# Performance work log

Measured on AMD Instinct MI355X. Metric: run time of the kernel, lower is better.

## Reference

```python
import jax, jax.numpy as jnp
import numpy as np

NUM_GROUPS = 32
EPS = 1e-6


def group_norm(x, gamma, beta):
    # x: [b, c, h, w]
    b, c, h, w = x.shape
    g = NUM_GROUPS
    xg = x.reshape(b, g, c // g, h, w)
    mean = xg.mean(axis=(2, 3, 4), keepdims=True)
    var = xg.var(axis=(2, 3, 4), keepdims=True)
    xn = ((xg - mean) * jax.lax.rsqrt(var + EPS)).reshape(b, c, h, w)
    return xn * gamma[None, :, None, None] + beta[None, :, None, None]


def conv1x1(x, w, b):
    # x: [b, c, h, w], w: [out_c, in_c], b: [out_c]
    return jnp.einsum('bchw,oc->bohw', x, w) + b[None, :, None, None]


def setup_inputs() -> dict:
    key = jax.random.key(0)
    ks = jax.random.split(key, 11)
    B, C, H, W = 4, 512, 64, 64
    s = 1.0 / np.sqrt(C)
    inp = {
        'x': jax.random.normal(ks[0], (B, C, H, W), dtype=jnp.float32),
        'gn_gamma': jnp.ones((C,), dtype=jnp.float32),
        'gn_beta': jnp.zeros((C,), dtype=jnp.float32),
        'wq': jax.random.normal(ks[1], (C, C), dtype=jnp.float32) * s,
        'bq': jax.random.normal(ks[2], (C,), dtype=jnp.float32) * 0.01,
        'wk': jax.random.normal(ks[3], (C, C), dtype=jnp.float32) * s,
        'bk': jax.random.normal(ks[4], (C,), dtype=jnp.float32) * 0.01,
        'wv': jax.random.normal(ks[5], (C, C), dtype=jnp.float32) * s,
        'bv': jax.random.normal(ks[6], (C,), dtype=jnp.float32) * 0.01,
        'wo': jax.random.normal(ks[7], (C, C), dtype=jnp.float32) * s,
        'bo': jax.random.normal(ks[8], (C,), dtype=jnp.float32) * 0.01,
    }
    return inp


def reference(x, gn_gamma, gn_beta, wq, bq, wk, bk, wv, bv, wo, bo):
    b, c, h, w = x.shape
    h_ = group_norm(x, gn_gamma, gn_beta)
    q = conv1x1(h_, wq, bq).reshape(b, c, h * w)  # [b, c, n]
    k = conv1x1(h_, wk, bk).reshape(b, c, h * w)
    v = conv1x1(h_, wv, bv).reshape(b, c, h * w)
    scale = jnp.asarray(c, x.dtype) ** -0.5
    # attn[b, i, j] = softmax_j(q_i . k_j * scale)
    attn = jax.nn.softmax(jnp.einsum('bci,bcj->bij', q, k) * scale, axis=-1)
    # A[b, c, i] = sum_j attn[b, i, j] * v[b, c, j]
    A = jnp.einsum('bij,bcj->bci', attn, v).reshape(b, c, h, w)
    A = conv1x1(A, wo, bo)
    # NOTE: the original module multiplies (not adds) the input by the attention output
    return x * A
```

## Files before the change

### kernel.cpp

```cpp
#include <hip/hip_runtime.h>
#include <hip/hip_bf16.h>
#include <stdint.h>

typedef __bf16 bf16x8 __attribute__((ext_vector_type(8)));
typedef __bf16 bf16x4 __attribute__((ext_vector_type(4)));
typedef float f32x4 __attribute__((ext_vector_type(4)));

__device__ __forceinline__ void gload_lds16(const __bf16* g, __bf16* l) {
  __builtin_amdgcn_global_load_lds(
      (const __attribute__((address_space(1))) void*)g,
      (__attribute__((address_space(3))) void*)l, 16, 0, 0);
}

__global__ __launch_bounds__(256) void cvt4_kernel(const float* __restrict__ s0,
                                                   const float* __restrict__ s1,
                                                   const float* __restrict__ s2,
                                                   const float* __restrict__ s3,
                                                   __bf16* __restrict__ dst) {
  int i = blockIdx.x * 256 + threadIdx.x;
  const float* srcs[4] = {s0, s1, s2, s3};
  int m = i >> 18;
  dst[i] = (__bf16)srcs[m][i & 262143];
}

__global__ __launch_bounds__(256) void biascat_kernel(const float* __restrict__ bq,
                                                      const float* __restrict__ bk,
                                                      float* __restrict__ bqk) {
  int i = blockIdx.x * 256 + threadIdx.x;
  bqk[i] = (i < 512) ? bq[i] : bk[i - 512];
}

__global__ __launch_bounds__(256) void gn1a_kernel(const float* __restrict__ x,
                                                   __bf16* __restrict__ xbf,
                                                   float2* __restrict__ part) {
  const int tid = threadIdx.x;
  const size_t base4 = ((size_t)blockIdx.x * 8192) >> 2;
  const float4* x4 = (const float4*)x;
  bf16x4* o4 = (bf16x4*)xbf;

  float s1 = 0.f, s2 = 0.f;
#pragma unroll
  for (int j = 0; j < 8; ++j) {
    float4 t = x4[base4 + tid + j * 256];
    s1 += t.x + t.y + t.z + t.w;
    s2 += t.x * t.x + t.y * t.y + t.z * t.z + t.w * t.w;
    bf16x4 o;
    o[0] = (__bf16)t.x; o[1] = (__bf16)t.y; o[2] = (__bf16)t.z; o[3] = (__bf16)t.w;
    o4[base4 + tid + j * 256] = o;
  }
#pragma unroll
  for (int off = 32; off; off >>= 1) {
    s1 += __shfl_xor(s1, off);
    s2 += __shfl_xor(s2, off);
  }
  __shared__ float r1[4], r2[4];
  if ((tid & 63) == 0) { r1[tid >> 6] = s1; r2[tid >> 6] = s2; }
  __syncthreads();
  if (tid == 0)
    part[blockIdx.x] = float2{r1[0] + r1[1] + r1[2] + r1[3],
                              r2[0] + r2[1] + r2[2] + r2[3]};
}

__global__ __launch_bounds__(512) void gn1b_kernel(const float2* __restrict__ part,
                                                   const float* __restrict__ gamma,
                                                   const float* __restrict__ beta,
                                                   float2* __restrict__ gmbt) {
  const int b = blockIdx.x;
  const int t = threadIdx.x;
  __shared__ float sm[32], si[32];
  if (t < 32) {
    float s1 = 0.f, s2 = 0.f;
#pragma unroll
    for (int j = 0; j < 8; ++j) {
      float2 p = part[(b * 32 + t) * 8 + j];
      s1 += p.x; s2 += p.y;
    }
    const float mean = s1 * (1.f / 65536.f);
    const float var = s2 * (1.f / 65536.f) - mean * mean;
    sm[t] = mean;
    si[t] = rsqrtf(var + 1e-6f);
  }
  __syncthreads();
  const int g = t >> 4;
  const float gm = gamma[t] * si[g];
  gmbt[b * 512 + t] = float2{gm, beta[t] - sm[g] * gm};
}

__global__ __launch_bounds__(256) void gn2_kernel(const __bf16* __restrict__ xbf,
                                                  const float2* __restrict__ gmbt,
                                                  __bf16* __restrict__ hnT) {
  const int b = blockIdx.z;
  const int c0 = blockIdx.y * 64;
  const int n0 = blockIdx.x * 64;
  const int t = threadIdx.x;
  __shared__ __bf16 tile[64][72];

  {
    const int row = t >> 2;
    const int col = (t & 3) * 16;
    const __bf16* src = xbf + ((size_t)(b * 512 + c0 + row)) * 4096 + n0 + col;
    bf16x8 u0 = *(const bf16x8*)src;
    bf16x8 u1 = *(const bf16x8*)(src + 8);
    *(bf16x8*)&tile[row][col] = u0;
    *(bf16x8*)&tile[row][col + 8] = u1;
  }
  __syncthreads();
  {
    const int nrow = t >> 2;
    const int cc = (t & 3) * 16;
    bf16x8 o0, o1;
#pragma unroll
    for (int j = 0; j < 16; ++j) {
      const int c = c0 + cc + j;
      float2 s = gmbt[b * 512 + c];
      float val = (float)tile[cc + j][nrow] * s.x + s.y;
      if (j < 8) o0[j] = (__bf16)val; else o1[j - 8] = (__bf16)val;
    }
    __bf16* dst = hnT + ((size_t)b * 4096 + n0 + nrow) * 512 + c0 + cc;
    *(bf16x8*)dst = o0;
    *(bf16x8*)(dst + 8) = o1;
  }
}

__global__ __launch_bounds__(256) void rowsum_inv_kernel(const __bf16* __restrict__ P,
                                                         float* __restrict__ inv) {
  const int r = blockIdx.x * 4 + (threadIdx.x >> 6);
  const int lane = threadIdx.x & 63;
  const bf16x8* rp = (const bf16x8*)(P + (size_t)r * 4096);
  float s = 0.f;
#pragma unroll
  for (int j = 0; j < 8; ++j) {
    bf16x8 v = rp[lane + j * 64];
#pragma unroll
    for (int e = 0; e < 8; ++e) s += (float)v[e];
  }
#pragma unroll
  for (int off = 32; off; off >>= 1) s += __shfl_xor(s, off);
  if (lane == 0) inv[r] = 1.0f / s;
}

template <int BIAS, int EEXP, int RSCALE, int KC>
__global__ __launch_bounds__(512) void gemm6r_kernel(
    const __bf16* __restrict__ A, int lda, long long sA,
    const __bf16* __restrict__ Bm, int ldb, long long sB,
    __bf16* __restrict__ Out, int ldo, long long sO,
    const float* __restrict__ bias, const float* __restrict__ rowinv,
    float scale) {
  constexpr int ASLOT = 8192;
  constexpr int BSLOT = 4096;
  constexpr int WN = 32;
  constexpr int BST = WN + 8;
  __shared__ __bf16 sm[6 * ASLOT + 6 * BSLOT];
  __bf16* smB = sm + 6 * ASLOT;

  const int gx = gridDim.x, gxy = gx * gridDim.y;
  const int nwg = gxy * gridDim.z;
  int bid = blockIdx.x + gx * blockIdx.y + gxy * blockIdx.z;
  bid = (bid & 7) * (nwg >> 3) + (bid >> 3);
  const int bz = bid / gxy;
  const int rem = bid - bz * gxy;
  const int by = rem / gx, bx = rem - by * gx;
  const int tm0 = by * 256, tn0 = bx * 128;

  const int t = threadIdx.x;
  const int lane = t & 63, wid = t >> 6;
  const int wr = wid >> 2, wc = wid & 3;

  const __bf16* Az = A + (size_t)bz * sA;
  const __bf16* Bz = Bm + (size_t)bz * sB;

  const int scol = ((t & 3) * 8) ^ (((t >> 3) & 3) * 8);
  const __bf16* gA0 = Az + (size_t)(tm0 + (t >> 2)) * lda + scol;
  const __bf16* gA1 = gA0 + (size_t)128 * lda;
  const __bf16* gB0 = Bz + (size_t)(tn0 + (t >> 2)) * ldb + scol;
  __bf16* dA = sm + t * 8;
  __bf16* dB = smB + t * 8;

  auto stageA = [&](int ks, int sl) {
    gload_lds16(gA0 + (size_t)ks * 32, dA + sl * ASLOT);
    gload_lds16(gA1 + (size_t)ks * 32, dA + sl * ASLOT + 4096);
  };
  auto stageB = [&](int ks, int sl) {
    gload_lds16(gB0 + (size_t)ks * 32, dB + sl * BSLOT);
  };

  const int lr = lane & 15;
  const int kb = ((lane >> 4) * 16) ^ ((lr & 6) << 3);
  const __bf16* rdA = sm + (((wr * 128 + lr) * 64 + kb) >> 1);
  const __bf16* rdB = smB + (((wc * WN + lr) * 64 + kb) >> 1);

  f32x4 acc[8][2];
#pragma unroll
  for (int m = 0; m < 8; ++m) {
    acc[m][0] = f32x4{0.f, 0.f, 0.f, 0.f};
    acc[m][1] = f32x4{0.f, 0.f, 0.f, 0.f};
  }
  bf16x8 av[8];

  auto rdAfr = [&](int sl) {
#pragma unroll
    for (int m = 0; m < 8; ++m)
      av[m] = *(const bf16x8*)(rdA + sl * ASLOT + m * 512);
  };
  auto mmaPh = [&](int sl, int nh) {
    bf16x8 bv = *(const bf16x8*)(rdB + sl * BSLOT + nh * 512);
    __builtin_amdgcn_s_barrier();
    __builtin_amdgcn_s_setprio(1);
#pragma unroll
    for (int m = 0; m < 8; ++m)
      acc[m][nh] = __builtin_amdgcn_mfma_f32_16x16x32_bf16(av[m], bv, acc[m][nh], 0, 0, 0);
    __builtin_amdgcn_s_setprio(0);
    __builtin_amdgcn_s_barrier();
  };

  constexpr int TOT = KC / 32;

  stageA(0, 0); stageB(0, 0);
  stageA(1, 1); stageB(1, 1);
  stageA(2, 2); stageB(2, 2);
  stageA(3, 3); stageB(3, 3);
  stageA(4, 4); stageB(4, 4);
  asm volatile("s_waitcnt vmcnt(12)" ::: "memory");
  __builtin_amdgcn_s_barrier();

  int cs = 0;
  int ss = 5;
#pragma unroll 1
  for (int s = 0; s < TOT - 5; ++s) {
    rdAfr(cs); stageA(s + 5, ss);   mmaPh(cs, 0);
    stageB(s + 5, ss);
    asm volatile("s_waitcnt vmcnt(12)" ::: "memory");
    mmaPh(cs, 1);
    cs = (cs == 5) ? 0 : cs + 1;
    ss = (ss == 5) ? 0 : ss + 1;
  }
  rdAfr(cs); mmaPh(cs, 0);
  asm volatile("s_waitcnt vmcnt(9)" ::: "memory");
  mmaPh(cs, 1); cs = (cs == 5) ? 0 : cs + 1;
  rdAfr(cs); mmaPh(cs, 0);
  asm volatile("s_waitcnt vmcnt(6)" ::: "memory");
  mmaPh(cs, 1); cs = (cs == 5) ? 0 : cs + 1;
  rdAfr(cs); mmaPh(cs, 0);
  asm volatile("s_waitcnt vmcnt(3)" ::: "memory");
  mmaPh(cs, 1); cs = (cs == 5) ? 0 : cs + 1;
  rdAfr(cs); mmaPh(cs, 0);
  asm volatile("s_waitcnt vmcnt(0)" ::: "memory");
  mmaPh(cs, 1); cs = (cs == 5) ? 0 : cs + 1;
  rdAfr(cs); mmaPh(cs, 0);
  mmaPh(cs, 1);

  __bf16* bnc = sm + wid * 16 * BST;
  const int q4 = (lane >> 4) * 4;
  const int row0 = tm0 + wr * 128;
  const int wn = tn0 + wc * WN;
  float bcol[2];
  bcol[0] = BIAS ? bias[wn + lr] : 0.f;
  bcol[1] = BIAS ? bias[wn + 16 + lr] : 0.f;
#pragma unroll
  for (int m = 0; m < 8; ++m) {
    float ri[4];
    if constexpr (RSCALE) {
#pragma unroll
      for (int r = 0; r < 4; ++r)
        ri[r] = rowinv[(size_t)bz * 4096 + row0 + m * 16 + q4 + r];
    }
#pragma unroll
    for (int n = 0; n < 2; ++n)
#pragma unroll
      for (int r = 0; r < 4; ++r) {
        float val = acc[m][n][r] * scale + bcol[n];
        if constexpr (EEXP) val = exp2f(val * 1.44269504f);
        if constexpr (RSCALE) val *= ri[r];
        bnc[(q4 + r) * BST + n * 16 + lr] = (__bf16)val;
      }
    const int rr = lane >> 2, c8 = (lane & 3) * 8;
    bf16x8 v0 = *(const bf16x8*)&bnc[rr * BST + c8];
    __bf16* op = Out + (size_t)bz * sO +
                 (size_t)(row0 + m * 16 + rr) * ldo + wn + c8;
    *(bf16x8*)op = v0;
  }
}

template <int EPI, int BIAS>
__global__ __launch_bounds__(256) void gemm_lds_kernel(
    const __bf16* __restrict__ A, int lda, long long sA,
    const __bf16* __restrict__ Bm, int ldb, long long sB,
    void* __restrict__ Out, int ldo, long long sO,
    const float* __restrict__ bias, const __bf16* __restrict__ xmul,
    long long sX, float scale, int K) {
  __shared__ __bf16 sTa[2][128 * 32];
  __shared__ __bf16 sTb[2][128 * 32];

  const int gx = gridDim.x, gxy = gx * gridDim.y;
  const int nwg = gxy * gridDim.z;
  int bid = blockIdx.x + gx * blockIdx.y + gxy * blockIdx.z;
  if ((nwg & 7) == 0) bid = (bid & 7) * (nwg >> 3) + (bid >> 3);
  const int bz = bid / gxy;
  const int rem = bid - bz * gxy;
  const int by = rem / gx;
  const int bx = rem - by * gx;

  const int tid = threadIdx.x;
  const int lane = tid & 63;
  const int wid = tid >> 6;
  const int wr = wid >> 1, wc = wid & 1;
  const int tm0 = by * 128, tn0 = bx * 128;
  const int lr = lane & 15, lk = (lane >> 4) * 8;

  const int ch0 = wid * 2;
  const int srow = lane >> 2;
  const int scol = (lane & 3) * 8;
  const __bf16* gA0 = A + (size_t)bz * sA + (size_t)(tm0 + ch0 * 16 + srow) * lda + scol;
  const __bf16* gB0 = Bm + (size_t)bz * sB + (size_t)(tn0 + ch0 * 16 + srow) * ldb + scol;
  const size_t stepA = (size_t)16 * lda, stepB = (size_t)16 * ldb;

  f32x4 acc[4][4];
#pragma unroll
  for (int i = 0; i < 4; ++i)
#pragma unroll
    for (int j = 0; j < 4; ++j) acc[i][j] = f32x4{0.f, 0.f, 0.f, 0.f};

  const int T = K >> 5;
  gload_lds16(gA0, &sTa[0][ch0 * 512]);
  gload_lds16(gA0 + stepA, &sTa[0][ch0 * 512 + 512]);
  gload_lds16(gB0, &sTb[0][ch0 * 512]);
  gload_lds16(gB0 + stepB, &sTb[0][ch0 * 512 + 512]);

  for (int tt = 0; tt < T; ++tt) {
    __syncthreads();
    const int cur = tt & 1;
    if (tt + 1 < T) {
      const __bf16* a = gA0 + (size_t)(tt + 1) * 32;
      const __bf16* b = gB0 + (size_t)(tt + 1) * 32;
      gload_lds16(a, &sTa[cur ^ 1][ch0 * 512]);
      gload_lds16(a + stepA, &sTa[cur ^ 1][ch0 * 512 + 512]);
      gload_lds16(b, &sTb[cur ^ 1][ch0 * 512]);
      gload_lds16(b + stepB, &sTb[cur ^ 1][ch0 * 512 + 512]);
    }
    const __bf16* fa = &sTa[cur][(wr * 64 + lr) * 32 + lk];
    const __bf16* fb = &sTb[cur][(wc * 64 + lr) * 32 + lk];
    bf16x8 a[4], b[4];
#pragma unroll
    for (int i = 0; i < 4; ++i) a[i] = *(const bf16x8*)(fa + i * 512);
#pragma unroll
    for (int j = 0; j < 4; ++j) b[j] = *(const bf16x8*)(fb + j * 512);
#pragma unroll
    for (int i = 0; i < 4; ++i)
#pragma unroll
      for (int j = 0; j < 4; ++j)
        acc[i][j] = __builtin_amdgcn_mfma_f32_16x16x32_bf16(a[i], b[j], acc[i][j], 0, 0, 0);
  }

  const int wm = tm0 + wr * 64, wn = tn0 + wc * 64;
#pragma unroll
  for (int i = 0; i < 4; ++i) {
#pragma unroll
    for (int r = 0; r < 4; ++r) {
      const int row = wm + i * 16 + (lane >> 4) * 4 + r;
#pragma unroll
      for (int j = 0; j < 4; ++j) {
        const int col = wn + j * 16 + lr;
        float val = acc[i][j][r] * scale;
        if (BIAS == 1) val += bias[col];
        if (BIAS == 2) val += bias[row];
        const size_t off = (size_t)bz * sO + (size_t)row * ldo + col;
        if (EPI == 0) {
          ((__bf16*)Out)[off] = (__bf16)val;
        } else if (EPI == 1) {
          ((float*)Out)[off] = val;
        } else {
          ((float*)Out)[off] = (float)xmul[(size_t)bz * sX + (size_t)row * ldo + col] * val;
        }
      }
    }
  }
}

extern "C" void kernel_launch(void* const* d_in, const int* in_sizes, int n_in,
                              void* d_out, int out_size, void* d_ws, size_t ws_size,
                              hipStream_t stream) {
  const int C = 512, N = 4096;
  const float* x = (const float*)d_in[0];
  const float* gng = (const float*)d_in[1];
  const float* gnb = (const float*)d_in[2];
  const float* wq = (const float*)d_in[3];
  const float* bq = (const float*)d_in[4];
  const float* wk = (const float*)d_in[5];
  const float* bk = (const float*)d_in[6];
  const float* wv = (const float*)d_in[7];
  const float* bv = (const float*)d_in[8];
  const float* wo = (const float*)d_in[9];
  const float* bo = (const float*)d_in[10];

  char* ws = (char*)d_ws;
  const size_t MB = 1ull << 20;
  const long long NC = (long long)N * C;
  const long long NN = (long long)N * N;
  const long long NQK = (long long)N * 1024;
  const bool batched = ws_size >= 194 * MB + 32768;

  __bf16 *S, *qkT, *a2T, *v, *xbf, *wqB;
  char* misc;
  if (batched) {
    S   = (__bf16*)(ws);
    qkT = (__bf16*)(ws + 128 * MB);
    a2T = qkT;
    v   = (__bf16*)(ws + 160 * MB);
    xbf = (__bf16*)(ws + 176 * MB);
    wqB = (__bf16*)(ws + 192 * MB);
    misc = ws + 194 * MB;
  } else {
    S   = (__bf16*)(ws);
    qkT = (__bf16*)(ws + 32 * MB);
    a2T = (__bf16*)(ws + 64 * MB);
    v   = (__bf16*)(ws + 80 * MB);
    xbf = (__bf16*)(ws + 96 * MB);
    wqB = (__bf16*)(ws + 112 * MB);
    misc = ws + 114 * MB;
  }
  __bf16* hnT = (__bf16*)ws;
  __bf16* wvB = wqB + 2 * 262144;
  __bf16* woB = wvB + 262144;
  float* bqk   = (float*)misc;
  float2* gmbt = (float2*)(misc + 4096);
  float2* part = (float2*)(misc + 20480);
  float* rowInv = (float*)d_out;

  const float scl = 0.044194173824159216f;

  cvt4_kernel<<<4096, 256, 0, stream>>>(wq, wk, wv, wo, wqB);
  biascat_kernel<<<4, 256, 0, stream>>>(bq, bk, bqk);
  gn1a_kernel<<<1024, 256, 0, stream>>>(x, xbf, part);
  gn1b_kernel<<<4, 512, 0, stream>>>(part, gng, gnb, gmbt);
  gn2_kernel<<<dim3(64, 8, 4), 256, 0, stream>>>(xbf, gmbt, hnT);

  gemm6r_kernel<1, 0, 0, 512><<<dim3(8, 16, 4), 512, 0, stream>>>(
      hnT, C, NC, wqB, C, 0, qkT, 1024, NQK, bqk, nullptr, 1.f);
  gemm_lds_kernel<0, 2><<<dim3(32, 4, 4), 256, 0, stream>>>(
      wvB, C, 0, hnT, C, NC, v, N, NC, bv, nullptr, 0, 1.f, C);

  if (batched) {
    gemm6r_kernel<0, 1, 0, 512><<<dim3(32, 16, 4), 512, 0, stream>>>(
        qkT, 1024, NQK, qkT + 512, 1024, NQK, S, N, NN, nullptr, nullptr, scl);
    rowsum_inv_kernel<<<4096, 256, 0, stream>>>(S, rowInv);
    gemm6r_kernel<0, 0, 1, 4096><<<dim3(4, 16, 4), 512, 0, stream>>>(
        S, N, NN, v, N, NC, a2T, C, NC, nullptr, rowInv, 1.f);
  } else {
    for (int b = 0; b < 4; ++b) {
      gemm6r_kernel<0, 1, 0, 512><<<dim3(32, 16, 1), 512, 0, stream>>>(
          qkT + (size_t)b * NQK, 1024, 0, qkT + (size_t)b * NQK + 512, 1024, 0,
          S, N, 0, nullptr, nullptr, scl);
      rowsum_inv_kernel<<<1024, 256, 0, stream>>>(S, rowInv);
      gemm6r_kernel<0, 0, 1, 4096><<<dim3(4, 16, 1), 512, 0, stream>>>(
          S, N, 0, v + (size_t)b * NC, N, 0, a2T + (size_t)b * NC, C, 0,
          nullptr, rowInv, 1.f);
    }
  }

  gemm_lds_kernel<2, 2><<<dim3(32, 4, 4), 256, 0, stream>>>(
      woB, C, 0, a2T, C, NC, (float*)d_out, N, NC, bo, xbf, NC, 1.f, C);
}
```

Before: 303.2 us.

## Replace 8-wave 256x128 GEMM with 4-wave 128x128 tile and 4-slot pipeline

Swaps the 512-thread GEMM (256x128 tile, 6-slot LDS ring, per-wave 128x32 output) for a 256-thread kernel with a 128x128 tile, a 4-slot LDS ring and per-wave 64x64 output using 4x4 MFMA blocks. Each wave now reuses its A and B fragments across 16 MFMAs, so fewer LDS reads are needed per MFMA. LDS use per block drops to 64KB, which may allow more resident blocks, and the grids double in the M direction. The trade-off is a shallower prefetch depth (3 stages in flight) and one barrier per k-step instead of two.

```diff
diff --git a/kernel.cpp b/kernel.cpp
--- a/kernel.cpp
+++ b/kernel.cpp
@@ -140,18 +140,16 @@
 }
 
 template <int BIAS, int EEXP, int RSCALE, int KC>
-__global__ __launch_bounds__(512) void gemm6r_kernel(
+__global__ __launch_bounds__(256) void gemm4w_kernel(
     const __bf16* __restrict__ A, int lda, long long sA,
     const __bf16* __restrict__ Bm, int ldb, long long sB,
     __bf16* __restrict__ Out, int ldo, long long sO,
     const float* __restrict__ bias, const float* __restrict__ rowinv,
     float scale) {
-  constexpr int ASLOT = 8192;
-  constexpr int BSLOT = 4096;
-  constexpr int WN = 32;
-  constexpr int BST = WN + 8;
-  __shared__ __bf16 sm[6 * ASLOT + 6 * BSLOT];
-  __bf16* smB = sm + 6 * ASLOT;
+  constexpr int SLOT = 4096;
+  constexpr int BST = 72;
+  __shared__ __bf16 sm[8 * SLOT];
+  __bf16* smB = sm + 4 * SLOT;
 
   const int gx = gridDim.x, gxy = gx * gridDim.y;
   const int nwg = gxy * gridDim.z;
@@ -160,104 +158,92 @@
   const int bz = bid / gxy;
   const int rem = bid - bz * gxy;
   const int by = rem / gx, bx = rem - by * gx;
-  const int tm0 = by * 256, tn0 = bx * 128;
+  const int tm0 = by * 128, tn0 = bx * 128;
 
   const int t = threadIdx.x;
   const int lane = t & 63, wid = t >> 6;
-  const int wr = wid >> 2, wc = wid & 3;
+  const int wr = wid >> 1, wc = wid & 1;
 
   const __bf16* Az = A + (size_t)bz * sA;
   const __bf16* Bz = Bm + (size_t)bz * sB;
 
   const int scol = ((t & 3) * 8) ^ (((t >> 3) & 3) * 8);
   const __bf16* gA0 = Az + (size_t)(tm0 + (t >> 2)) * lda + scol;
-  const __bf16* gA1 = gA0 + (size_t)128 * lda;
+  const __bf16* gA1 = gA0 + (size_t)64 * lda;
   const __bf16* gB0 = Bz + (size_t)(tn0 + (t >> 2)) * ldb + scol;
+  const __bf16* gB1 = gB0 + (size_t)64 * ldb;
   __bf16* dA = sm + t * 8;
   __bf16* dB = smB + t * 8;
 
-  auto stageA = [&](int ks, int sl) {
-    gload_lds16(gA0 + (size_t)ks * 32, dA + sl * ASLOT);
-    gload_lds16(gA1 + (size_t)ks * 32, dA + sl * ASLOT + 4096);
-  };
-  auto stageB = [&](int ks, int sl) {
-    gload_lds16(gB0 + (size_t)ks * 32, dB + sl * BSLOT);
+  auto stage = [&](int ks) {
+    const int sl = ks & 3;
+    gload_lds16(gA0 + (size_t)ks * 32, dA + sl * SLOT);
+    gload_lds16(gA1 + (size_t)ks * 32, dA + sl * SLOT + 2048);
+    gload_lds16(gB0 + (size_t)ks * 32, dB + sl * SLOT);
+    gload_lds16(gB1 + (size_t)ks * 32, dB + sl * SLOT + 2048);
   };
 
   const int lr = lane & 15;
   const int kb = ((lane >> 4) * 16) ^ ((lr & 6) << 3);
-  const __bf16* rdA = sm + (((wr * 128 + lr) * 64 + kb) >> 1);
-  const __bf16* rdB = smB + (((wc * WN + lr) * 64 + kb) >> 1);
-
-  f32x4 acc[8][2];
-#pragma unroll
-  for (int m = 0; m < 8; ++m) {
-    acc[m][0] = f32x4{0.f, 0.f, 0.f, 0.f};
-    acc[m][1] = f32x4{0.f, 0.f, 0.f, 0.f};
-  }
-  bf16x8 av[8];
-
-  auto rdAfr = [&](int sl) {
-#pragma unroll
-    for (int m = 0; m < 8; ++m)
-      av[m] = *(const bf16x8*)(rdA + sl * ASLOT + m * 512);
+  const __bf16* rdA = sm + (((wr * 64 + lr) * 64 + kb) >> 1);
+  const __bf16* rdB = smB + (((wc * 64 + lr) * 64 + kb) >> 1);
+
+  f32x4 acc[4][4];
+#pragma unroll
+  for (int i = 0; i < 4; ++i)
+#pragma unroll
+    for (int j = 0; j < 4; ++j) acc[i][j] = f32x4{0.f, 0.f, 0.f, 0.f};
+  bf16x8 av[4], bv[4];
+
+  auto rdfr = [&](int sl) {
+#pragma unroll
+    for (int m = 0; m < 4; ++m) av[m] = *(const bf16x8*)(rdA + sl * SLOT + m * 512);
+#pragma unroll
+    for (int n = 0; n < 4; ++n) bv[n] = *(const bf16x8*)(rdB + sl * SLOT + n * 512);
   };
-  auto mmaPh = [&](int sl, int nh) {
-    bf16x8 bv = *(const bf16x8*)(rdB + sl * BSLOT + nh * 512);
+  auto mma16 = [&] {
     __builtin_amdgcn_s_barrier();
     __builtin_amdgcn_s_setprio(1);
 #pragma unroll
-    for (int m = 0; m < 8; ++m)
-      acc[m][nh] = __builtin_amdgcn_mfma_f32_16x16x32_bf16(av[m], bv, acc[m][nh], 0, 0, 0);
+    for (int m = 0; m < 4; ++m)
+#pragma unroll
+      for (int n = 0; n < 4; ++n)
+        acc[m][n] = __builtin_amdgcn_mfma_f32_16x16x32_bf16(av[m], bv[n], acc[m][n], 0, 0, 0);
     __builtin_amdgcn_s_setprio(0);
+  };
+
+  constexpr int TOT = KC / 32;
+
+  stage(0); stage(1); stage(2);
+  asm volatile("s_waitcnt vmcnt(8)" ::: "memory");
+  __builtin_amdgcn_s_barrier();
+
+#pragma unroll 1
+  for (int s = 0; s < TOT - 3; ++s) {
+    rdfr(s & 3);
+    stage(s + 3);
+    mma16();
+    asm volatile("s_waitcnt vmcnt(8)" ::: "memory");
     __builtin_amdgcn_s_barrier();
-  };
-
-  constexpr int TOT = KC / 32;
-
-  stageA(0, 0); stageB(0, 0);
-  stageA(1, 1); stageB(1, 1);
-  stageA(2, 2); stageB(2, 2);
-  stageA(3, 3); stageB(3, 3);
-  stageA(4, 4); stageB(4, 4);
-  asm volatile("s_waitcnt vmcnt(12)" ::: "memory");
+  }
+  rdfr((TOT - 3) & 3); mma16();
+  asm volatile("s_waitcnt vmcnt(4)" ::: "memory");
   __builtin_amdgcn_s_barrier();
-
-  int cs = 0;
-  int ss = 5;
-#pragma unroll 1
-  for (int s = 0; s < TOT - 5; ++s) {
-    rdAfr(cs); stageA(s + 5, ss);   mmaPh(cs, 0);
-    stageB(s + 5, ss);
-    asm volatile("s_waitcnt vmcnt(12)" ::: "memory");
-    mmaPh(cs, 1);
-    cs = (cs == 5) ? 0 : cs + 1;
-    ss = (ss == 5) ? 0 : ss + 1;
-  }
-  rdAfr(cs); mmaPh(cs, 0);
-  asm volatile("s_waitcnt vmcnt(9)" ::: "memory");
-  mmaPh(cs, 1); cs = (cs == 5) ? 0 : cs + 1;
-  rdAfr(cs); mmaPh(cs, 0);
-  asm volatile("s_waitcnt vmcnt(6)" ::: "memory");
-  mmaPh(cs, 1); cs = (cs == 5) ? 0 : cs + 1;
-  rdAfr(cs); mmaPh(cs, 0);
-  asm volatile("s_waitcnt vmcnt(3)" ::: "memory");
-  mmaPh(cs, 1); cs = (cs == 5) ? 0 : cs + 1;
-  rdAfr(cs); mmaPh(cs, 0);
+  rdfr((TOT - 2) & 3); mma16();
   asm volatile("s_waitcnt vmcnt(0)" ::: "memory");
-  mmaPh(cs, 1); cs = (cs == 5) ? 0 : cs + 1;
-  rdAfr(cs); mmaPh(cs, 0);
-  mmaPh(cs, 1);
+  __builtin_amdgcn_s_barrier();
+  rdfr((TOT - 1) & 3); mma16();
+  __builtin_amdgcn_s_barrier();
 
   __bf16* bnc = sm + wid * 16 * BST;
   const int q4 = (lane >> 4) * 4;
-  const int row0 = tm0 + wr * 128;
-  const int wn = tn0 + wc * WN;
-  float bcol[2];
-  bcol[0] = BIAS ? bias[wn + lr] : 0.f;
-  bcol[1] = BIAS ? bias[wn + 16 + lr] : 0.f;
-#pragma unroll
-  for (int m = 0; m < 8; ++m) {
+  const int row0 = tm0 + wr * 64;
+  const int wn = tn0 + wc * 64;
+  float bcol[4];
+#pragma unroll
+  for (int n = 0; n < 4; ++n) bcol[n] = BIAS ? bias[wn + n * 16 + lr] : 0.f;
+#pragma unroll
+  for (int m = 0; m < 4; ++m) {
     float ri[4];
     if constexpr (RSCALE) {
 #pragma unroll
@@ -265,7 +251,7 @@
         ri[r] = rowinv[(size_t)bz * 4096 + row0 + m * 16 + q4 + r];
     }
 #pragma unroll
-    for (int n = 0; n < 2; ++n)
+    for (int n = 0; n < 4; ++n)
 #pragma unroll
       for (int r = 0; r < 4; ++r) {
         float val = acc[m][n][r] * scale + bcol[n];
@@ -273,11 +259,13 @@
         if constexpr (RSCALE) val *= ri[r];
         bnc[(q4 + r) * BST + n * 16 + lr] = (__bf16)val;
       }
-    const int rr = lane >> 2, c8 = (lane & 3) * 8;
+    const int rr = lane >> 3, c8 = (lane & 7) * 8;
     bf16x8 v0 = *(const bf16x8*)&bnc[rr * BST + c8];
+    bf16x8 v1 = *(const bf16x8*)&bnc[(rr + 8) * BST + c8];
     __bf16* op = Out + (size_t)bz * sO +
                  (size_t)(row0 + m * 16 + rr) * ldo + wn + c8;
     *(bf16x8*)op = v0;
+    *(bf16x8*)(op + (size_t)8 * ldo) = v1;
   }
 }
 
@@ -434,24 +422,24 @@
   gn1b_kernel<<<4, 512, 0, stream>>>(part, gng, gnb, gmbt);
   gn2_kernel<<<dim3(64, 8, 4), 256, 0, stream>>>(xbf, gmbt, hnT);
 
-  gemm6r_kernel<1, 0, 0, 512><<<dim3(8, 16, 4), 512, 0, stream>>>(
+  gemm4w_kernel<1, 0, 0, 512><<<dim3(8, 32, 4), 256, 0, stream>>>(
       hnT, C, NC, wqB, C, 0, qkT, 1024, NQK, bqk, nullptr, 1.f);
   gemm_lds_kernel<0, 2><<<dim3(32, 4, 4), 256, 0, stream>>>(
       wvB, C, 0, hnT, C, NC, v, N, NC, bv, nullptr, 0, 1.f, C);
 
   if (batched) {
-    gemm6r_kernel<0, 1, 0, 512><<<dim3(32, 16, 4), 512, 0, stream>>>(
+    gemm4w_kernel<0, 1, 0, 512><<<dim3(32, 32, 4), 256, 0, stream>>>(
         qkT, 1024, NQK, qkT + 512, 1024, NQK, S, N, NN, nullptr, nullptr, scl);
     rowsum_inv_kernel<<<4096, 256, 0, stream>>>(S, rowInv);
-    gemm6r_kernel<0, 0, 1, 4096><<<dim3(4, 16, 4), 512, 0, stream>>>(
+    gemm4w_kernel<0, 0, 1, 4096><<<dim3(4, 32, 4), 256, 0, stream>>>(
         S, N, NN, v, N, NC, a2T, C, NC, nullptr, rowInv, 1.f);
   } else {
     for (int b = 0; b < 4; ++b) {
-      gemm6r_kernel<0, 1, 0, 512><<<dim3(32, 16, 1), 512, 0, stream>>>(
+      gemm4w_kernel<0, 1, 0, 512><<<dim3(32, 32, 1), 256, 0, stream>>>(
           qkT + (size_t)b * NQK, 1024, 0, qkT + (size_t)b * NQK + 512, 1024, 0,
           S, N, 0, nullptr, nullptr, scl);
       rowsum_inv_kernel<<<1024, 256, 0, stream>>>(S, rowInv);
-      gemm6r_kernel<0, 0, 1, 4096><<<dim3(4, 16, 1), 512, 0, stream>>>(
+      gemm4w_kernel<0, 0, 1, 4096><<<dim3(4, 32, 1), 256, 0, stream>>>(
           S, N, 0, v + (size_t)b * NC, N, 0, a2T + (size_t)b * NC, C, 0,
           nullptr, rowInv, 1.f);
     }
```

Result: faster. 289.1 us (-4.6%).
